# Performance work log

Measured on AMD Instinct MI355X. Metric: run time of the kernel, lower is better.

The kernel has to match this reference:

```python
import jax, jax.numpy as jnp
import numpy as np

B, S, D = 2, 1024, 4096
HQ, HKV, HD = 32, 8, 128
GROUPS = HQ // HKV          # 4
SCALE = HD ** -0.5


def _rope_tables(key):
    # standard RoPE cos/sin tables, non-interleaved (half-split) layout
    inv_freq = 1.0 / (10000.0 ** (jnp.arange(0, HD, 2, dtype=jnp.float32) / HD))  # [HD/2]
    pos = jnp.arange(S, dtype=jnp.float32)                                        # [S]
    freqs = pos[:, None] * inv_freq[None, :]                                      # [S, HD/2]
    emb = jnp.concatenate([freqs, freqs], axis=-1)                                # [S, HD]
    cos = jnp.broadcast_to(jnp.cos(emb)[None], (B, S, HD))
    sin = jnp.broadcast_to(jnp.sin(emb)[None], (B, S, HD))
    return cos, sin


def setup_inputs() -> dict:
    key = jax.random.key(0)
    ks = jax.random.split(key, 6)
    hidden_states = jax.random.normal(ks[0], (B, S, D), dtype=jnp.float32)
    cos_table, sin_table = _rope_tables(ks[1])
    Wq = jax.random.normal(ks[2], (D, HQ * HD), dtype=jnp.float32) * (D ** -0.5)
    Wk = jax.random.normal(ks[3], (D, HKV * HD), dtype=jnp.float32) * (D ** -0.5)
    Wv = jax.random.normal(ks[4], (D, HKV * HD), dtype=jnp.float32) * (D ** -0.5)
    Wo = jax.random.normal(ks[5], (HQ * HD, D), dtype=jnp.float32) * ((HQ * HD) ** -0.5)
    return {"hidden_states": hidden_states, "cos_table": cos_table,
            "sin_table": sin_table, "Wq": Wq, "Wk": Wk, "Wv": Wv, "Wo": Wo}


def _rotate_half(x):
    x1, x2 = jnp.split(x, 2, axis=-1)
    return jnp.concatenate([-x2, x1], axis=-1)


def _apply_rope(x, cos, sin):
    # x: [B, S, H, HD]; cos/sin: [B, S, HD] broadcast across heads
    c = cos[:, :, None, :]
    s = sin[:, :, None, :]
    return x * c + _rotate_half(x) * s


def reference(hidden_states, cos_table, sin_table, Wq, Wk, Wv, Wo):
    b, s, _ = hidden_states.shape
    # QKV projections (no bias, Llama-style)
    q = (hidden_states @ Wq).reshape(b, s, HQ, HD)
    k = (hidden_states @ Wk).reshape(b, s, HKV, HD)
    v = (hidden_states @ Wv).reshape(b, s, HKV, HD)
    # fused RoPE on q and k (in [B, S, H, HD] layout, as in source)
    q = _apply_rope(q, cos_table, sin_table)
    k = _apply_rope(k, cos_table, sin_table)
    # -> [B, H, S, HD]
    q = q.transpose(0, 2, 1, 3)
    k = k.transpose(0, 2, 1, 3)
    v = v.transpose(0, 2, 1, 3)
    # GQA repeat_kv: [B, HKV, S, HD] -> [B, HQ, S, HD]
    k = jnp.repeat(k, GROUPS, axis=1)
    v = jnp.repeat(v, GROUPS, axis=1)
    # SDPA, no mask (source calls sdpa without a mask)
    scores = jnp.einsum('bhqd,bhkd->bhqk', q, k) * SCALE
    attn = jax.nn.softmax(scores, axis=-1)
    out = jnp.einsum('bhqk,bhkd->bhqd', attn, v)
    out = out.transpose(0, 2, 1, 3).reshape(b, s, HQ * HD)
    return out @ Wo
```

## Files before the change

### kernel.cpp

```cpp
#include <hip/hip_runtime.h>

#define B_   2
#define S_   1024
#define D_   4096
#define HQ_  32
#define HKV_ 8
#define HD_  128
#define SCALE_ 0.08838834764831845f

typedef unsigned short u16;
typedef __attribute__((ext_vector_type(8))) short s16x8;
typedef __attribute__((ext_vector_type(4))) short s16x4;
typedef __attribute__((ext_vector_type(4))) float f32x4;

#define MFMA(a,b,c) __builtin_amdgcn_mfma_f32_16x16x32_bf16((a),(b),(c),0,0,0)

__device__ __forceinline__ u16 bf16_rne(float x) {
  unsigned u = __float_as_uint(x);
  u += 0x7fffu + ((u >> 16) & 1u);
  return (u16)(u >> 16);
}
__device__ __forceinline__ float bf16_up(u16 h) {
  return __uint_as_float(((unsigned)h) << 16);
}
__device__ __forceinline__ void split2(float x, u16& h, u16& l) {
  h = bf16_rne(x);
  l = bf16_rne(x - bf16_up(h));
}

__device__ __forceinline__ void cvt_hi_lo(float a, float b, unsigned& hi, unsigned& lo) {
  unsigned h, l;
  asm("v_cvt_pk_bf16_f32 %0, %1, %2" : "=v"(h) : "v"(a), "v"(b));
  float ra = __uint_as_float(h << 16);
  float rb = __uint_as_float(h & 0xffff0000u);
  float la = a - ra, lb = b - rb;
  asm("v_cvt_pk_bf16_f32 %0, %1, %2" : "=v"(l) : "v"(la), "v"(lb));
  hi = h; lo = l;
}
__device__ __forceinline__ void pack8(float4 x, float4 y, uint4& h, uint4& l) {
  unsigned h0,h1,h2,h3,l0,l1,l2,l3;
  cvt_hi_lo(x.x, x.y, h0, l0);
  cvt_hi_lo(x.z, x.w, h1, l1);
  cvt_hi_lo(y.x, y.y, h2, l2);
  cvt_hi_lo(y.z, y.w, h3, l3);
  h = make_uint4(h0,h1,h2,h3); l = make_uint4(l0,l1,l2,l3);
}

typedef const __attribute__((address_space(1))) void* gas_ptr;
typedef __attribute__((address_space(3))) void* las_ptr;
__device__ __forceinline__ void gload_lds16(const void* g, void* l) {
  __builtin_amdgcn_global_load_lds((gas_ptr)g, (las_ptr)l, 16, 0, 0);
}

__global__ __launch_bounds__(256) void frag_b2(
    const float* __restrict__ W, u16* __restrict__ dh, u16* __restrict__ dl,
    int N, int n0, int Ntot16, int ntoff)
{
  __shared__ float T[32][68];
  const int kt = blockIdx.x, nbk = blockIdx.y;
  const int tid = threadIdx.x;
#pragma unroll
  for (int rep = 0; rep < 2; ++rep) {
    int idx = tid + rep * 256;
    int row = idx >> 4, c4 = (idx & 15) * 4;
    float4 v = *reinterpret_cast<const float4*>(&W[(size_t)(kt*32 + row) * N + n0 + nbk*64 + c4]);
    *reinterpret_cast<float4*>(&T[row][c4]) = v;
  }
  __syncthreads();
  int c = tid;
  int nt = c >> 6, l = c & 63;
  const size_t base = (((size_t)(kt >> 1) * Ntot16 + ntoff + nbk*4 + nt) * 2 + (kt & 1)) * 512;
  u16 hh[8], ll[8];
#pragma unroll
  for (int j = 0; j < 8; ++j) split2(T[(l >> 4)*8 + j][nt*16 + (l & 15)], hh[j], ll[j]);
  *reinterpret_cast<s16x8*>(&dh[base + (size_t)l * 8]) =
    (s16x8){(short)hh[0],(short)hh[1],(short)hh[2],(short)hh[3],
            (short)hh[4],(short)hh[5],(short)hh[6],(short)hh[7]};
  *reinterpret_cast<s16x8*>(&dl[base + (size_t)l * 8]) =
    (s16x8){(short)ll[0],(short)ll[1],(short)ll[2],(short)ll[3],
            (short)ll[4],(short)ll[5],(short)ll[6],(short)ll[7]};
}

__global__ __launch_bounds__(256) void frag_a(
    const float* __restrict__ src, u16* __restrict__ dh, u16* __restrict__ dl)
{
  __shared__ float T[128][68];
  const int kt = blockIdx.x;
  const int mb = blockIdx.y;
  const int tid = threadIdx.x;
#pragma unroll
  for (int rep = 0; rep < 8; ++rep) {
    int idx = tid + rep * 256;
    int row = idx >> 4, c4 = (idx & 15) * 4;
    float4 v = *reinterpret_cast<const float4*>(&src[(size_t)(mb*128 + row) * 4096 + kt*64 + c4]);
    *reinterpret_cast<float4*>(&T[row][c4]) = v;
  }
  __syncthreads();
#pragma unroll
  for (int rep = 0; rep < 4; ++rep) {
    int c = tid + rep * 256;
    int mt = c >> 7, rem = c & 127, kk = rem >> 6, l = rem & 63;
    u16 hh[8], ll[8];
#pragma unroll
    for (int j = 0; j < 8; ++j)
      split2(T[mt*16 + (l & 15)][kk*32 + (l >> 4)*8 + j], hh[j], ll[j]);
    size_t off = (((size_t)(kt*128 + mb*8 + mt)) * 2 + kk) * 512 + (size_t)l * 8;
    *reinterpret_cast<s16x8*>(&dh[off]) =
      (s16x8){(short)hh[0],(short)hh[1],(short)hh[2],(short)hh[3],
              (short)hh[4],(short)hh[5],(short)hh[6],(short)hh[7]};
    *reinterpret_cast<s16x8*>(&dl[off]) =
      (s16x8){(short)ll[0],(short)ll[1],(short)ll[2],(short)ll[3],
              (short)ll[4],(short)ll[5],(short)ll[6],(short)ll[7]};
  }
}

template<int NF, bool RQ>
__device__ __forceinline__ void gemm128_core(
    const u16* __restrict__ PAh, const u16* __restrict__ PAl,
    const u16* __restrict__ PBh, const u16* __restrict__ PBl,
    float* __restrict__ C0, float* __restrict__ C1, float* __restrict__ C2,
    int ldc0, int Nt16, int mb, int nb, u16* L)
{
  const int tid  = threadIdx.x;
  const int lane = tid & 63;
  const int wid  = tid >> 6;
  const int loff = lane * 8;
  const int wm4  = (wid >> 2) * 4;
  const int wnf  = (wid & 3) * NF;
  constexpr int BNT  = 4 * NF;
  constexpr int NCHW = 2 + NF;

  u16* A0 = L;
  u16* A1 = L + 8192;
  u16* B0 = L + 16384;
  u16* B1 = L + 16384 + BNT*1024;

  f32x4 acc[4][NF];
#pragma unroll
  for (int i = 0; i < 4; ++i)
#pragma unroll
    for (int j = 0; j < NF; ++j) acc[i][j] = (f32x4){0.f,0.f,0.f,0.f};

  const u16* sp[NCHW];
  int   dlo[NCHW];
  int   dadd[NCHW];
  size_t adv2[NCHW];
  const size_t aSlab = 131072;
  const size_t bSlab = (size_t)Nt16 * 1024;
#pragma unroll
  for (int i = 0; i < NCHW; ++i) {
    int c = wid + 8*i;
    if (c < 8) {
      sp[i]  = PAh + (size_t)(mb*8 + c)*1024 + loff;
      dlo[i] = c*512;             dadd[i] = 8192;      adv2[i] = aSlab - 512;
    } else if (c < 16) {
      int m = c - 8;
      sp[i]  = PAl + (size_t)(mb*8 + m)*1024 + loff;
      dlo[i] = 4096 + m*512;      dadd[i] = 8192;      adv2[i] = aSlab - 512;
    } else if (c < 16 + BNT) {
      int n = c - 16;
      sp[i]  = PBh + (size_t)(nb*BNT + n)*1024 + loff;
      dlo[i] = 16384 + n*512;     dadd[i] = BNT*1024;  adv2[i] = bSlab - 512;
    } else {
      int n = c - 16 - BNT;
      sp[i]  = PBl + (size_t)(nb*BNT + n)*1024 + loff;
      dlo[i] = 16384 + BNT*512 + n*512; dadd[i] = BNT*1024; adv2[i] = bSlab - 512;
    }
  }

#pragma unroll
  for (int i = 0; i < NCHW; ++i) {
    gload_lds16(sp[i], L + dlo[i]);
    sp[i] += 512;
  }
  __syncthreads();

  for (int t = 0; t < 128; ++t) {
    u16* la = (t & 1) ? A1 : A0;
    u16* lb = (t & 1) ? B1 : B0;
    if (t < 127) {
      const int p = (t + 1) & 1;
#pragma unroll
      for (int i = 0; i < NCHW; ++i) {
        gload_lds16(sp[i], L + dlo[i] + (p ? dadd[i] : 0));
        sp[i] += p ? adv2[i] : 512;
      }
    }

    s16x8 ah[4], al[4], bh[NF], bl[NF];
#pragma unroll
    for (int mf = 0; mf < 4; ++mf)
      ah[mf] = *reinterpret_cast<const s16x8*>(&la[(wm4+mf)*512 + loff]);
#pragma unroll
    for (int nf = 0; nf < NF; ++nf)
      bh[nf] = *reinterpret_cast<const s16x8*>(&lb[(wnf+nf)*512 + loff]);
    __builtin_amdgcn_s_setprio(1);
#pragma unroll
    for (int nf = 0; nf < NF; ++nf)
#pragma unroll
      for (int mf = 0; mf < 4; ++mf)
        acc[mf][nf] = MFMA(ah[mf], bh[nf], acc[mf][nf]);
    __builtin_amdgcn_s_setprio(0);
#pragma unroll
    for (int mf = 0; mf < 4; ++mf)
      al[mf] = *reinterpret_cast<const s16x8*>(&la[4096 + (wm4+mf)*512 + loff]);
    __builtin_amdgcn_s_setprio(1);
#pragma unroll
    for (int nf = 0; nf < NF; ++nf)
#pragma unroll
      for (int mf = 0; mf < 4; ++mf)
        acc[mf][nf] = MFMA(al[mf], bh[nf], acc[mf][nf]);
    __builtin_amdgcn_s_setprio(0);
#pragma unroll
    for (int nf = 0; nf < NF; ++nf)
      bl[nf] = *reinterpret_cast<const s16x8*>(&lb[BNT*512 + (wnf+nf)*512 + loff]);
    __builtin_amdgcn_s_setprio(1);
#pragma unroll
    for (int nf = 0; nf < NF; ++nf)
#pragma unroll
      for (int mf = 0; mf < 4; ++mf)
        acc[mf][nf] = MFMA(ah[mf], bl[nf], acc[mf][nf]);
    __builtin_amdgcn_s_setprio(0);
    __syncthreads();
  }

  const int lg = lane >> 4, lr = lane & 15;
  const int rowb = mb*128 + (wid >> 2) * 64;
#pragma unroll
  for (int mf = 0; mf < 4; ++mf)
#pragma unroll
    for (int nf = 0; nf < NF; ++nf)
#pragma unroll
      for (int r = 0; r < 4; ++r) {
        int row = rowb + mf*16 + lg*4 + r;
        float v = acc[mf][nf][r];
        int gcol = nb*(NF*64) + (wid & 3)*(NF*16) + nf*16 + lr;
        if constexpr (RQ) {
          if (gcol < 4096)      C0[(size_t)row * 4096 + gcol] = v;
          else if (gcol < 5120) C1[(size_t)row * 1024 + (gcol - 4096)] = v;
          else                  C2[(size_t)row * 1024 + (gcol - 5120)] = v;
        } else {
          C0[(size_t)row * ldc0 + gcol] = v;
        }
      }
}

__global__ __launch_bounds__(512, 4) void gemm_qkv3(
    const u16* __restrict__ XAh, const u16* __restrict__ XAl,
    const u16* __restrict__ WBh, const u16* __restrict__ WBl,
    float* __restrict__ qb, float* __restrict__ kb, float* __restrict__ vb)
{
  __shared__ __attribute__((aligned(16))) u16 L[40960];
  int id = blockIdx.x;
  int xcd = id & 7, c = id >> 3;
  int nb = xcd * 4 + (c >> 4);
  int mb = c & 15;
  gemm128_core<3, true>(XAh, XAl, WBh, WBl, qb, kb, vb, 0, 384, mb, nb, L);
}

__global__ __launch_bounds__(512, 4) void gemm_out3(
    const u16* __restrict__ ABh, const u16* __restrict__ ABl,
    const u16* __restrict__ WOh, const u16* __restrict__ WOl,
    float* __restrict__ outp)
{
  __shared__ __attribute__((aligned(16))) u16 L[32768];
  int id = blockIdx.x;
  int xcd = id & 7, c = id >> 3;
  int nb = xcd * 4 + (c >> 4);
  int mb = c & 15;
  gemm128_core<2, false>(ABh, ABl, WOh, WOl, outp, nullptr, nullptr,
                         4096, 256, mb, nb, L);
}

template<int NF, bool RQ>
__device__ __forceinline__ void gemm256_core(
    const u16* __restrict__ PAh, const u16* __restrict__ PAl,
    const u16* __restrict__ PBh, const u16* __restrict__ PBl,
    float* __restrict__ C0, float* __restrict__ C1, float* __restrict__ C2,
    int ldc0, int Nt16, int mb, int nb, int k0, int nk, u16* L)
{
  const int tid  = threadIdx.x;
  const int lane = tid & 63;
  const int wid  = tid >> 6;
  const int loff = lane * 8;
  const int wm8  = (wid >> 2) * 8;
  const int wnf  = (wid & 3) * NF;

  u16* A0 = L;
  u16* A1 = L + 16384;
  u16* B0 = L + 32768;
  u16* B1 = L + 32768 + NF*4096;

  f32x4 acc[8][NF];
#pragma unroll
  for (int i = 0; i < 8; ++i)
#pragma unroll
    for (int j = 0; j < NF; ++j) acc[i][j] = (f32x4){0.f,0.f,0.f,0.f};

  auto STAGE = [&](int t, u16* la_, u16* lb_) {
    const int kt64 = t >> 1, kk = t & 1;
    const size_t aSlab = (size_t)kt64 * 131072;
    const size_t bSlab = (size_t)kt64 * ((size_t)Nt16 * 1024);
    const int NCH = 32 + 8*NF;
#pragma unroll
    for (int c = wid; c < NCH; c += 8) {
      const u16* src; u16* dst;
      if (c < 16) {
        src = PAh + aSlab + (((size_t)(mb*16 + c))*2 + kk)*512;
        dst = la_ + c*512;
      } else if (c < 32) {
        int m = c - 16;
        src = PAl + aSlab + (((size_t)(mb*16 + m))*2 + kk)*512;
        dst = la_ + 8192 + m*512;
      } else if (c < 32 + 4*NF) {
        int n = c - 32;
        src = PBh + bSlab + (((size_t)(nb*4*NF + n))*2 + kk)*512;
        dst = lb_ + n*512;
      } else {
        int n = c - 32 - 4*NF;
        src = PBl + bSlab + (((size_t)(nb*4*NF + n))*2 + kk)*512;
        dst = lb_ + NF*2048 + n*512;
      }
      gload_lds16(src + loff, dst);
    }
  };

  STAGE(k0, (k0 & 1) ? A1 : A0, (k0 & 1) ? B1 : B0);
  __syncthreads();

  for (int t = k0; t < k0 + nk; ++t) {
    u16* la = (t & 1) ? A1 : A0;
    u16* lb = (t & 1) ? B1 : B0;
    if (t + 1 < k0 + nk)
      STAGE(t + 1, (t & 1) ? A0 : A1, (t & 1) ? B0 : B1);

    s16x8 ah[8], al[8], bh[NF], bl[NF];
#pragma unroll
    for (int mf = 0; mf < 8; ++mf)
      ah[mf] = *reinterpret_cast<const s16x8*>(&la[(wm8+mf)*512 + loff]);
#pragma unroll
    for (int nf = 0; nf < NF; ++nf)
      bh[nf] = *reinterpret_cast<const s16x8*>(&lb[(wnf+nf)*512 + loff]);
    __builtin_amdgcn_s_setprio(1);
#pragma unroll
    for (int nf = 0; nf < NF; ++nf)
#pragma unroll
      for (int mf = 0; mf < 8; ++mf)
        acc[mf][nf] = MFMA(ah[mf], bh[nf], acc[mf][nf]);
    __builtin_amdgcn_s_setprio(0);
#pragma unroll
    for (int mf = 0; mf < 8; ++mf)
      al[mf] = *reinterpret_cast<const s16x8*>(&la[8192 + (wm8+mf)*512 + loff]);
    __builtin_amdgcn_s_setprio(1);
#pragma unroll
    for (int nf = 0; nf < NF; ++nf)
#pragma unroll
      for (int mf = 0; mf < 8; ++mf)
        acc[mf][nf] = MFMA(al[mf], bh[nf], acc[mf][nf]);
    __builtin_amdgcn_s_setprio(0);
#pragma unroll
    for (int nf = 0; nf < NF; ++nf)
      bl[nf] = *reinterpret_cast<const s16x8*>(&lb[NF*2048 + (wnf+nf)*512 + loff]);
    __builtin_amdgcn_s_setprio(1);
#pragma unroll
    for (int nf = 0; nf < NF; ++nf)
#pragma unroll
      for (int mf = 0; mf < 8; ++mf)
        acc[mf][nf] = MFMA(ah[mf], bl[nf], acc[mf][nf]);
    __builtin_amdgcn_s_setprio(0);
    __syncthreads();
  }

  const int lg = lane >> 4, lr = lane & 15;
  const int rowb = mb*256 + (wid >> 2) * 128;
#pragma unroll
  for (int mf = 0; mf < 8; ++mf)
#pragma unroll
    for (int nf = 0; nf < NF; ++nf)
#pragma unroll
      for (int r = 0; r < 4; ++r) {
        int row = rowb + mf*16 + lg*4 + r;
        float v = acc[mf][nf][r];
        if constexpr (RQ) {
          int gcol = nb*(NF*64) + (wid & 3)*(NF*16) + nf*16 + lr;
          if (gcol < 4096)      C0[(size_t)row * 4096 + gcol] = v;
          else if (gcol < 5120) C1[(size_t)row * 1024 + (gcol - 4096)] = v;
          else                  C2[(size_t)row * 1024 + (gcol - 5120)] = v;
        } else {
          int col = nb*(NF*64) + (wid & 3)*(NF*16) + nf*16 + lr;
          C0[(size_t)row * ldc0 + col] = v;
        }
      }
}

__global__ __launch_bounds__(512) void gemm_qkv2(
    const u16* __restrict__ XAh, const u16* __restrict__ XAl,
    const u16* __restrict__ WA,
    float* __restrict__ qb, float* __restrict__ kb, float* __restrict__ vb)
{
  __shared__ __attribute__((aligned(16))) u16 L[65536];
  int id = blockIdx.x;
  int swz = (id & 7) * 24 + (id >> 3);
  const u16 *Bh, *Bl; float* C; int ldc, Nt16, mb, nb;
  if (swz < 128)      { Bh = WA;          Bl = WA+16777216; C = qb; ldc = 4096; Nt16 = 256; mb = swz & 7;  nb = swz >> 3; }
  else if (swz < 160) { int u = swz-128; Bh = WA+33554432; Bl = WA+37748736; C = kb; ldc = 1024; Nt16 = 64; mb = u & 7; nb = u >> 3; }
  else                { int u = swz-160; Bh = WA+41943040; Bl = WA+46137344; C = vb; ldc = 1024; Nt16 = 64; mb = u & 7; nb = u >> 3; }
  gemm256_core<4, false>(XAh, XAl, Bh, Bl, C, nullptr, nullptr, ldc, Nt16, mb, nb, 0, 128, L);
}

__global__ __launch_bounds__(512) void gemm_out2(
    const u16* __restrict__ ABh, const u16* __restrict__ ABl,
    const u16* __restrict__ WOh, const u16* __restrict__ WOl,
    float* __restrict__ outp, float* __restrict__ c2)
{
  __shared__ __attribute__((aligned(16))) u16 L[65536];
  int id = blockIdx.x;
  int swz = (id & 7) * 32 + (id >> 3);
  int u = swz & 127, s = swz >> 7;
  int mb = u & 7, nb = u >> 3;
  gemm256_core<4, false>(ABh, ABl, WOh, WOl, s ? c2 : outp, nullptr, nullptr,
                         4096, 256, mb, nb, s*64, 64, L);
}

__global__ __launch_bounds__(256) void add_out(
    float* __restrict__ o, const float* __restrict__ c2)
{
  int i = blockIdx.x * 256 + threadIdx.x;
  float4 a = reinterpret_cast<float4*>(o)[i];
  float4 b = reinterpret_cast<const float4*>(c2)[i];
  a.x += b.x; a.y += b.y; a.z += b.z; a.w += b.w;
  reinterpret_cast<float4*>(o)[i] = a;
}

__global__ __launch_bounds__(256) void frag_kv(
    const float* __restrict__ kb, const float* __restrict__ vb,
    const float* __restrict__ cosT, const float* __restrict__ sinT,
    u16* __restrict__ KFh, u16* __restrict__ KFl,
    u16* __restrict__ VFh, u16* __restrict__ VFl)
{
  __shared__ float T[32][132];
  const int bid  = blockIdx.x;
  const int isV  = bid >> 9;
  const int bkvh = (bid >> 5) & 15;
  const int chnk = bid & 31;
  const int tid  = threadIdx.x;
  const int b    = bkvh >> 3, kvh = bkvh & 7;

  const float* src = isV ? vb : kb;
  {
    int r0 = tid >> 5, c4 = (tid & 31) * 4;
    float sgn = (c4 < 64) ? -1.f : 1.f;
#pragma unroll
    for (int it = 0; it < 4; ++it) {
      int row = r0 + it * 8;
      int srow = chnk*32 + row;
      const float* rp = &src[(((size_t)(b * S_ + srow)) * HKV_ + kvh) * HD_];
      float4 v = *reinterpret_cast<const float4*>(rp + c4);
      if (!isV) {
        float4 p  = *reinterpret_cast<const float4*>(rp + (c4 ^ 64));
        float4 cc = *reinterpret_cast<const float4*>(&cosT[((size_t)(b*S_ + srow))*HD_ + c4]);
        float4 ss = *reinterpret_cast<const float4*>(&sinT[((size_t)(b*S_ + srow))*HD_ + c4]);
        v.x = v.x*cc.x + sgn*p.x*ss.x;
        v.y = v.y*cc.y + sgn*p.y*ss.y;
        v.z = v.z*cc.z + sgn*p.z*ss.z;
        v.w = v.w*cc.w + sgn*p.w*ss.w;
      }
      *reinterpret_cast<float4*>(&T[row][c4]) = v;
    }
  }
  __syncthreads();
#pragma unroll
  for (int rep = 0; rep < 2; ++rep) {
    int c2 = tid + rep * 256;
    int l = c2 & 63;
    u16 hh[8], ll[8];
    if (!isV) {
      int f = c2 >> 6, st_loc = f >> 2, dt = f & 3;
#pragma unroll
      for (int j = 0; j < 8; ++j)
        split2(T[st_loc*16 + (l & 15)][dt*32 + (l >> 4)*8 + j], hh[j], ll[j]);
      size_t off = ((size_t)bkvh*64 + chnk*2) * 2048 + (size_t)c2 * 8;
      *reinterpret_cast<s16x8*>(&KFh[off]) =
        (s16x8){(short)hh[0],(short)hh[1],(short)hh[2],(short)hh[3],
                (short)hh[4],(short)hh[5],(short)hh[6],(short)hh[7]};
      *reinterpret_cast<s16x8*>(&KFl[off]) =
        (s16x8){(short)ll[0],(short)ll[1],(short)ll[2],(short)ll[3],
                (short)ll[4],(short)ll[5],(short)ll[6],(short)ll[7]};
    } else {
      int dt16 = c2 >> 6;
#pragma unroll
      for (int j = 0; j < 8; ++j)
        split2(T[(l >> 4)*8 + j][dt16*16 + (l & 15)], hh[j], ll[j]);
      size_t off = ((size_t)bkvh*32 + chnk) * 4096 + (size_t)c2 * 8;
      *reinterpret_cast<s16x8*>(&VFh[off]) =
        (s16x8){(short)hh[0],(short)hh[1],(short)hh[2],(short)hh[3],
                (short)hh[4],(short)hh[5],(short)hh[6],(short)hh[7]};
      *reinterpret_cast<s16x8*>(&VFl[off]) =
        (s16x8){(short)ll[0],(short)ll[1],(short)ll[2],(short)ll[3],
                (short)ll[4],(short)ll[5],(short)ll[6],(short)ll[7]};
    }
  }
}

__global__ __launch_bounds__(512) void attn3(
    const float* __restrict__ qb,
    const float* __restrict__ cosT, const float* __restrict__ sinT,
    const u16* __restrict__ KFh, const u16* __restrict__ KFl,
    const u16* __restrict__ VFh, const u16* __restrict__ VFl,
    float* __restrict__ ob)
{
  __shared__ __attribute__((aligned(16))) u16 Klds[16384];
  __shared__ __attribute__((aligned(16))) u16 Vlds[16384];
  __shared__ u16 Ph[8][16][68], Pl[8][16][68];

  const int tid  = threadIdx.x;
  const int lane = tid & 63;
  const int wid  = tid >> 6;
  const int lr   = lane & 15;
  const int lg   = lane >> 4;
  const int loff = lane * 8;
  const int qt   = blockIdx.x;
  const int bh   = blockIdx.y;
  const int b    = bh >> 5, h = bh & 31;
  const int bkvh = b * 8 + (h >> 2);

  s16x8 qh[4], ql[4];
  {
    const int qrow = qt * 128 + wid * 16 + lr;
    const float* qp = qb + ((size_t)((b * S_ + qrow) * HQ_ + h)) * HD_;
    const float* cp = cosT + ((size_t)(b * S_ + qrow)) * HD_;
    const float* sp = sinT + ((size_t)(b * S_ + qrow)) * HD_;
#pragma unroll
    for (int kc = 0; kc < 4; ++kc) {
      const int d0 = kc * 32 + lg * 8;
      const float sgn = (d0 < 64) ? -1.f : 1.f;
      float4 v0 = *reinterpret_cast<const float4*>(qp + d0);
      float4 v1 = *reinterpret_cast<const float4*>(qp + d0 + 4);
      float4 p0 = *reinterpret_cast<const float4*>(qp + (d0 ^ 64));
      float4 p1 = *reinterpret_cast<const float4*>(qp + (d0 ^ 64) + 4);
      float4 c0 = *reinterpret_cast<const float4*>(cp + d0);
      float4 c1 = *reinterpret_cast<const float4*>(cp + d0 + 4);
      float4 s0 = *reinterpret_cast<const float4*>(sp + d0);
      float4 s1 = *reinterpret_cast<const float4*>(sp + d0 + 4);
      float4 r0, r1;
      r0.x = v0.x*c0.x + sgn*p0.x*s0.x;  r0.y = v0.y*c0.y + sgn*p0.y*s0.y;
      r0.z = v0.z*c0.z + sgn*p0.z*s0.z;  r0.w = v0.w*c0.w + sgn*p0.w*s0.w;
      r1.x = v1.x*c1.x + sgn*p1.x*s1.x;  r1.y = v1.y*c1.y + sgn*p1.y*s1.y;
      r1.z = v1.z*c1.z + sgn*p1.z*s1.z;  r1.w = v1.w*c1.w + sgn*p1.w*s1.w;
      uint4 h4, l4; pack8(r0, r1, h4, l4);
      qh[kc] = *reinterpret_cast<s16x8*>(&h4);
      ql[kc] = *reinterpret_cast<s16x8*>(&l4);
    }
  }

  f32x4 acc_o[8];
#pragma unroll
  for (int df = 0; df < 8; ++df) acc_o[df] = (f32x4){0.f, 0.f, 0.f, 0.f};
  float m_run[4] = {-1e30f, -1e30f, -1e30f, -1e30f};
  float l_run[4] = {0.f, 0.f, 0.f, 0.f};

  const u16* gKh = KFh + (size_t)bkvh * 131072;
  const u16* gKl = KFl + (size_t)bkvh * 131072;
  const u16* gVh = VFh + (size_t)bkvh * 131072;
  const u16* gVl = VFl + (size_t)bkvh * 131072;

#pragma unroll
  for (int i = 0; i < 4; ++i) {
    int idx = wid * 4 + i;
    const u16* src = (idx < 16) ? (gKh + idx*512) : (gKl + (idx-16)*512);
    u16* dst = Klds + ((idx < 16) ? idx*512 : 8192 + (idx-16)*512);
    gload_lds16(src + loff, dst);
  }
  __syncthreads();

  for (int t = 0; t < 16; ++t) {
#pragma unroll
    for (int i = 0; i < 4; ++i) {
      int idx = wid * 4 + i;
      const u16* src = (idx < 16) ? (gVh + t*8192 + idx*512)
                                  : (gVl + t*8192 + (idx-16)*512);
      u16* dst = Vlds + ((idx < 16) ? idx*512 : 8192 + (idx-16)*512);
      gload_lds16(src + loff, dst);
    }

    f32x4 accs[4];
#pragma unroll
    for (int nf = 0; nf < 4; ++nf) {
      accs[nf] = (f32x4){0.f, 0.f, 0.f, 0.f};
      s16x8 kh8[4], kl8[4];
#pragma unroll
      for (int kc = 0; kc < 4; ++kc) {
        kh8[kc] = *reinterpret_cast<const s16x8*>(&Klds[nf*2048 + kc*512 + loff]);
        kl8[kc] = *reinterpret_cast<const s16x8*>(&Klds[8192 + nf*2048 + kc*512 + loff]);
      }
#pragma unroll
      for (int kc = 0; kc < 4; ++kc) {
        accs[nf] = MFMA(qh[kc], kh8[kc], accs[nf]);
        accs[nf] = MFMA(ql[kc], kh8[kc], accs[nf]);
        accs[nf] = MFMA(qh[kc], kl8[kc], accs[nf]);
      }
    }
#pragma unroll
    for (int nf = 0; nf < 4; ++nf) accs[nf] *= SCALE_;

    float corr[4], rsum[4];
#pragma unroll
    for (int r = 0; r < 4; ++r) {
      float t0 = fmaxf(fmaxf(accs[0][r], accs[1][r]), fmaxf(accs[2][r], accs[3][r]));
      t0 = fmaxf(t0, __shfl_xor(t0, 1));
      t0 = fmaxf(t0, __shfl_xor(t0, 2));
      t0 = fmaxf(t0, __shfl_xor(t0, 4));
      t0 = fmaxf(t0, __shfl_xor(t0, 8));
      float mnew = fmaxf(m_run[r], t0);
      corr[r] = __expf(m_run[r] - mnew);
      m_run[r] = mnew;
      rsum[r] = 0.f;
    }
#pragma unroll
    for (int nf = 0; nf < 4; ++nf)
#pragma unroll
      for (int r = 0; r < 4; ++r) {
        float p = __expf(accs[nf][r] - m_run[r]);
        rsum[r] += p;
        u16 ph, pl;
        split2(p, ph, pl);
        Ph[wid][lg*4 + r][nf*16 + lr] = ph;
        Pl[wid][lg*4 + r][nf*16 + lr] = pl;
      }
#pragma unroll
    for (int r = 0; r < 4; ++r) {
      float s = rsum[r];
      s += __shfl_xor(s, 1); s += __shfl_xor(s, 2);
      s += __shfl_xor(s, 4); s += __shfl_xor(s, 8);
      l_run[r] = l_run[r] * corr[r] + s;
    }
#pragma unroll
    for (int df = 0; df < 8; ++df)
#pragma unroll
      for (int r = 0; r < 4; ++r) acc_o[df][r] *= corr[r];

    __syncthreads();

    if (t < 15) {
#pragma unroll
      for (int i = 0; i < 4; ++i) {
        int idx = wid * 4 + i;
        const u16* src = (idx < 16) ? (gKh + (t+1)*8192 + idx*512)
                                    : (gKl + (t+1)*8192 + (idx-16)*512);
        u16* dst = Klds + ((idx < 16) ? idx*512 : 8192 + (idx-16)*512);
        gload_lds16(src + loff, dst);
      }
    }

    s16x8 pa_h[2], pa_l[2];
#pragma unroll
    for (int kc = 0; kc < 2; ++kc) {
      pa_h[kc] = *reinterpret_cast<const s16x8*>(&Ph[wid][lr][kc*32 + lg*8]);
      pa_l[kc] = *reinterpret_cast<const s16x8*>(&Pl[wid][lr][kc*32 + lg*8]);
    }
#pragma unroll
    for (int df = 0; df < 8; ++df) {
      s16x8 vh8[2], vl8[2];
#pragma unroll
      for (int kc = 0; kc < 2; ++kc) {
        vh8[kc] = *reinterpret_cast<const s16x8*>(&Vlds[kc*4096 + df*512 + loff]);
        vl8[kc] = *reinterpret_cast<const s16x8*>(&Vlds[8192 + kc*4096 + df*512 + loff]);
      }
#pragma unroll
      for (int kc = 0; kc < 2; ++kc) {
        acc_o[df] = MFMA(pa_h[kc], vh8[kc], acc_o[df]);
        acc_o[df] = MFMA(pa_l[kc], vh8[kc], acc_o[df]);
        acc_o[df] = MFMA(pa_h[kc], vl8[kc], acc_o[df]);
      }
    }
    __syncthreads();
  }

  float inv_l[4];
#pragma unroll
  for (int r = 0; r < 4; ++r) inv_l[r] = 1.f / l_run[r];
#pragma unroll
  for (int df = 0; df < 8; ++df)
#pragma unroll
    for (int r = 0; r < 4; ++r) {
      int row = qt * 128 + wid * 16 + lg * 4 + r;
      ob[((size_t)((b * S_ + row) * HQ_ + h)) * HD_ + df*16 + lr] = acc_o[df][r] * inv_l[r];
    }
}

extern "C" void kernel_launch(void* const* d_in, const int* in_sizes, int n_in,
                              void* d_out, int out_size, void* d_ws, size_t ws_size,
                              hipStream_t stream)
{
  const float* hs   = (const float*)d_in[0];
  const float* cosT = (const float*)d_in[1];
  const float* sinT = (const float*)d_in[2];
  const float* Wq   = (const float*)d_in[3];
  const float* Wk   = (const float*)d_in[4];
  const float* Wv   = (const float*)d_in[5];
  const float* Wo   = (const float*)d_in[6];
  float* out = (float*)d_out;

  float* qb = (float*)d_ws;
  float* kb = qb + 8388608;
  float* vb = kb + 2097152;
  float* ab = vb + 2097152;
  u16*   FR = (u16*)(ab + 8388608);

  const size_t WS212 = 222298112ULL;

  if (ws_size >= WS212) {
    u16* XAh = FR;
    u16* XAl = FR + 8388608;
    u16* WBh = FR + 16777216;
    u16* WBl = FR + 41943040;
    u16* KFh = FR + 16777216;
    u16* KFl = FR + 18874368;
    u16* VFh = FR + 20971520;
    u16* VFl = FR + 23068672;
    u16* WOh = FR + 25165824;
    u16* WOl = FR + 41943040;

    frag_a<<<dim3(64,16), 256, 0, stream>>>(hs, XAh, XAl);
    frag_b2<<<dim3(128,64), 256, 0, stream>>>(Wq, WBh, WBl, 4096, 0, 384, 0);
    frag_b2<<<dim3(128,16), 256, 0, stream>>>(Wk, WBh, WBl, 1024, 0, 384, 256);
    frag_b2<<<dim3(128,16), 256, 0, stream>>>(Wv, WBh, WBl, 1024, 0, 384, 320);
    gemm_qkv3<<<512, 512, 0, stream>>>(XAh, XAl, WBh, WBl, qb, kb, vb);
    frag_kv<<<1024, 256, 0, stream>>>(kb, vb, cosT, sinT, KFh, KFl, VFh, VFl);
    frag_b2<<<dim3(128,64), 256, 0, stream>>>(Wo, WOh, WOl, 4096, 0, 256, 0);
    attn3<<<dim3(8, 64), 512, 0, stream>>>(qb, cosT, sinT, KFh, KFl, VFh, VFl, ab);
    frag_a<<<dim3(64,16), 256, 0, stream>>>(ab, XAh, XAl);
    gemm_out3<<<512, 512, 0, stream>>>(XAh, XAl, WOh, WOl, out);
  } else {
    u16* XAh = FR;
    u16* XAl = FR + 8388608;
    u16* WA  = FR + 16777216;
    frag_a<<<dim3(64,16), 256, 0, stream>>>(hs, XAh, XAl);
    frag_b2<<<dim3(128,64), 256, 0, stream>>>(Wq, WA,           WA+16777216, 4096, 0, 256, 0);
    frag_b2<<<dim3(128,16), 256, 0, stream>>>(Wk, WA+33554432,  WA+37748736, 1024, 0, 64, 0);
    frag_b2<<<dim3(128,16), 256, 0, stream>>>(Wv, WA+41943040,  WA+46137344, 1024, 0, 64, 0);
    gemm_qkv2<<<192, 512, 0, stream>>>(XAh, XAl, WA, qb, kb, vb);
    frag_kv<<<1024, 256, 0, stream>>>(kb, vb, cosT, sinT,
                                      WA, WA+2097152, WA+4194304, WA+6291456);
    frag_b2<<<dim3(128,64), 256, 0, stream>>>(Wo, WA+8388608, WA+25165824, 4096, 0, 256, 0);
    attn3<<<dim3(8, 64), 512, 0, stream>>>(qb, cosT, sinT,
                                           WA, WA+2097152, WA+4194304, WA+6291456, ab);
    frag_a<<<dim3(64,16), 256, 0, stream>>>(ab, XAh, XAl);
    gemm_out2<<<256, 512, 0, stream>>>(XAh, XAl, WA+8388608, WA+25165824, out, qb);
    add_out<<<8192, 256, 0, stream>>>(out, qb);
  }
}
```

Baseline: 648.3 us.

## Add smaller-tile attention kernel with 32-key steps and pairwise bf16 split packing

Introduces attn4, which handles 64 query rows per block with 4 waves and iterates over 32-key chunks using half-size LDS buffers. This gives more blocks (1024 instead of 512) and higher occupancy via launch_bounds(256,3), at the cost of twice as many loop iterations and barriers. The fragment conversion kernels now convert pairs of floats into packed hi/lo bf16 words with cvt_hi_lo and store them as uint4 instead of assembling eight shorts. attn4 replaces attn3 in the primary launch path, while the fallback path still uses attn3.

```diff
diff --git a/kernel.cpp b/kernel.cpp
--- a/kernel.cpp
+++ b/kernel.cpp
@@ -70,15 +70,13 @@
   int c = tid;
   int nt = c >> 6, l = c & 63;
   const size_t base = (((size_t)(kt >> 1) * Ntot16 + ntoff + nbk*4 + nt) * 2 + (kt & 1)) * 512;
-  u16 hh[8], ll[8];
-#pragma unroll
-  for (int j = 0; j < 8; ++j) split2(T[(l >> 4)*8 + j][nt*16 + (l & 15)], hh[j], ll[j]);
-  *reinterpret_cast<s16x8*>(&dh[base + (size_t)l * 8]) =
-    (s16x8){(short)hh[0],(short)hh[1],(short)hh[2],(short)hh[3],
-            (short)hh[4],(short)hh[5],(short)hh[6],(short)hh[7]};
-  *reinterpret_cast<s16x8*>(&dl[base + (size_t)l * 8]) =
-    (s16x8){(short)ll[0],(short)ll[1],(short)ll[2],(short)ll[3],
-            (short)ll[4],(short)ll[5],(short)ll[6],(short)ll[7]};
+  const int r0 = (l >> 4) * 8, cc = nt*16 + (l & 15);
+  unsigned hh4[4], ll4[4];
+#pragma unroll
+  for (int p = 0; p < 4; ++p)
+    cvt_hi_lo(T[r0 + 2*p][cc], T[r0 + 2*p + 1][cc], hh4[p], ll4[p]);
+  *reinterpret_cast<uint4*>(&dh[base + (size_t)l * 8]) = make_uint4(hh4[0],hh4[1],hh4[2],hh4[3]);
+  *reinterpret_cast<uint4*>(&dl[base + (size_t)l * 8]) = make_uint4(ll4[0],ll4[1],ll4[2],ll4[3]);
 }
 
 __global__ __launch_bounds__(256) void frag_a(
@@ -100,17 +98,14 @@
   for (int rep = 0; rep < 4; ++rep) {
     int c = tid + rep * 256;
     int mt = c >> 7, rem = c & 127, kk = rem >> 6, l = rem & 63;
-    u16 hh[8], ll[8];
-#pragma unroll
-    for (int j = 0; j < 8; ++j)
-      split2(T[mt*16 + (l & 15)][kk*32 + (l >> 4)*8 + j], hh[j], ll[j]);
+    const int rr = mt*16 + (l & 15), c0 = kk*32 + (l >> 4)*8;
+    unsigned hh4[4], ll4[4];
+#pragma unroll
+    for (int p = 0; p < 4; ++p)
+      cvt_hi_lo(T[rr][c0 + 2*p], T[rr][c0 + 2*p + 1], hh4[p], ll4[p]);
     size_t off = (((size_t)(kt*128 + mb*8 + mt)) * 2 + kk) * 512 + (size_t)l * 8;
-    *reinterpret_cast<s16x8*>(&dh[off]) =
-      (s16x8){(short)hh[0],(short)hh[1],(short)hh[2],(short)hh[3],
-              (short)hh[4],(short)hh[5],(short)hh[6],(short)hh[7]};
-    *reinterpret_cast<s16x8*>(&dl[off]) =
-      (s16x8){(short)ll[0],(short)ll[1],(short)ll[2],(short)ll[3],
-              (short)ll[4],(short)ll[5],(short)ll[6],(short)ll[7]};
+    *reinterpret_cast<uint4*>(&dh[off]) = make_uint4(hh4[0],hh4[1],hh4[2],hh4[3]);
+    *reinterpret_cast<uint4*>(&dl[off]) = make_uint4(ll4[0],ll4[1],ll4[2],ll4[3]);
   }
 }
 
@@ -473,45 +468,39 @@
   for (int rep = 0; rep < 2; ++rep) {
     int c2 = tid + rep * 256;
     int l = c2 & 63;
-    u16 hh[8], ll[8];
+    unsigned hh4[4], ll4[4];
     if (!isV) {
       int f = c2 >> 6, st_loc = f >> 2, dt = f & 3;
-#pragma unroll
-      for (int j = 0; j < 8; ++j)
-        split2(T[st_loc*16 + (l & 15)][dt*32 + (l >> 4)*8 + j], hh[j], ll[j]);
+      const int rr = st_loc*16 + (l & 15), c0 = dt*32 + (l >> 4)*8;
+#pragma unroll
+      for (int p = 0; p < 4; ++p)
+        cvt_hi_lo(T[rr][c0 + 2*p], T[rr][c0 + 2*p + 1], hh4[p], ll4[p]);
       size_t off = ((size_t)bkvh*64 + chnk*2) * 2048 + (size_t)c2 * 8;
-      *reinterpret_cast<s16x8*>(&KFh[off]) =
-        (s16x8){(short)hh[0],(short)hh[1],(short)hh[2],(short)hh[3],
-                (short)hh[4],(short)hh[5],(short)hh[6],(short)hh[7]};
-      *reinterpret_cast<s16x8*>(&KFl[off]) =
-        (s16x8){(short)ll[0],(short)ll[1],(short)ll[2],(short)ll[3],
-                (short)ll[4],(short)ll[5],(short)ll[6],(short)ll[7]};
+      *reinterpret_cast<uint4*>(&KFh[off]) = make_uint4(hh4[0],hh4[1],hh4[2],hh4[3]);
+      *reinterpret_cast<uint4*>(&KFl[off]) = make_uint4(ll4[0],ll4[1],ll4[2],ll4[3]);
     } else {
       int dt16 = c2 >> 6;
-#pragma unroll
-      for (int j = 0; j < 8; ++j)
-        split2(T[(l >> 4)*8 + j][dt16*16 + (l & 15)], hh[j], ll[j]);
+      const int r0 = (l >> 4)*8, cc = dt16*16 + (l & 15);
+#pragma unroll
+      for (int p = 0; p < 4; ++p)
+        cvt_hi_lo(T[r0 + 2*p][cc], T[r0 + 2*p + 1][cc], hh4[p], ll4[p]);
       size_t off = ((size_t)bkvh*32 + chnk) * 4096 + (size_t)c2 * 8;
-      *reinterpret_cast<s16x8*>(&VFh[off]) =
-        (s16x8){(short)hh[0],(short)hh[1],(short)hh[2],(short)hh[3],
-                (short)hh[4],(short)hh[5],(short)hh[6],(short)hh[7]};
-      *reinterpret_cast<s16x8*>(&VFl[off]) =
-        (s16x8){(short)ll[0],(short)ll[1],(short)ll[2],(short)ll[3],
-                (short)ll[4],(short)ll[5],(short)ll[6],(short)ll[7]};
-    }
-  }
-}
-
-__global__ __launch_bounds__(512) void attn3(
+      *reinterpret_cast<uint4*>(&VFh[off]) = make_uint4(hh4[0],hh4[1],hh4[2],hh4[3]);
+      *reinterpret_cast<uint4*>(&VFl[off]) = make_uint4(ll4[0],ll4[1],ll4[2],ll4[3]);
+    }
+  }
+}
+
+__global__ __launch_bounds__(256, 3) void attn4(
     const float* __restrict__ qb,
     const float* __restrict__ cosT, const float* __restrict__ sinT,
     const u16* __restrict__ KFh, const u16* __restrict__ KFl,
     const u16* __restrict__ VFh, const u16* __restrict__ VFl,
     float* __restrict__ ob)
 {
-  __shared__ __attribute__((aligned(16))) u16 Klds[16384];
-  __shared__ __attribute__((aligned(16))) u16 Vlds[16384];
-  __shared__ u16 Ph[8][16][68], Pl[8][16][68];
+  __shared__ __attribute__((aligned(16))) u16 Klds[8192];
+  __shared__ __attribute__((aligned(16))) u16 Vlds[8192];
+  __shared__ u16 Ph[4][16][36], Pl[4][16][36];
 
   const int tid  = threadIdx.x;
   const int lane = tid & 63;
@@ -526,7 +515,7 @@
 
   s16x8 qh[4], ql[4];
   {
-    const int qrow = qt * 128 + wid * 16 + lr;
+    const int qrow = qt * 64 + wid * 16 + lr;
     const float* qp = qb + ((size_t)((b * S_ + qrow) * HQ_ + h)) * HD_;
     const float* cp = cosT + ((size_t)(b * S_ + qrow)) * HD_;
     const float* sp = sinT + ((size_t)(b * S_ + qrow)) * HD_;
@@ -565,6 +554,176 @@
   const u16* gVl = VFl + (size_t)bkvh * 131072;
 
 #pragma unroll
+  for (int i = 0; i < 2; ++i) {
+    int c = wid * 2 + i;
+    gload_lds16(gKh + c*512 + loff, Klds + c*512);
+    gload_lds16(gKl + c*512 + loff, Klds + 4096 + c*512);
+  }
+  __syncthreads();
+
+  for (int t = 0; t < 32; ++t) {
+#pragma unroll
+    for (int i = 0; i < 2; ++i) {
+      int c = wid * 2 + i;
+      gload_lds16(gVh + t*4096 + c*512 + loff, Vlds + c*512);
+      gload_lds16(gVl + t*4096 + c*512 + loff, Vlds + 4096 + c*512);
+    }
+
+    f32x4 accs[2];
+#pragma unroll
+    for (int nf = 0; nf < 2; ++nf) {
+      accs[nf] = (f32x4){0.f, 0.f, 0.f, 0.f};
+      s16x8 kh8[4], kl8[4];
+#pragma unroll
+      for (int kc = 0; kc < 4; ++kc) {
+        kh8[kc] = *reinterpret_cast<const s16x8*>(&Klds[nf*2048 + kc*512 + loff]);
+        kl8[kc] = *reinterpret_cast<const s16x8*>(&Klds[4096 + nf*2048 + kc*512 + loff]);
+      }
+#pragma unroll
+      for (int kc = 0; kc < 4; ++kc) {
+        accs[nf] = MFMA(qh[kc], kh8[kc], accs[nf]);
+        accs[nf] = MFMA(ql[kc], kh8[kc], accs[nf]);
+        accs[nf] = MFMA(qh[kc], kl8[kc], accs[nf]);
+      }
+    }
+#pragma unroll
+    for (int nf = 0; nf < 2; ++nf) accs[nf] *= SCALE_;
+
+    float corr[4], rsum[4];
+#pragma unroll
+    for (int r = 0; r < 4; ++r) {
+      float t0 = fmaxf(accs[0][r], accs[1][r]);
+      t0 = fmaxf(t0, __shfl_xor(t0, 1));
+      t0 = fmaxf(t0, __shfl_xor(t0, 2));
+      t0 = fmaxf(t0, __shfl_xor(t0, 4));
+      t0 = fmaxf(t0, __shfl_xor(t0, 8));
+      float mnew = fmaxf(m_run[r], t0);
+      corr[r] = __expf(m_run[r] - mnew);
+      m_run[r] = mnew;
+      rsum[r] = 0.f;
+    }
+#pragma unroll
+    for (int nf = 0; nf < 2; ++nf)
+#pragma unroll
+      for (int r = 0; r < 4; ++r) {
+        float p = __expf(accs[nf][r] - m_run[r]);
+        rsum[r] += p;
+        u16 ph, pl;
+        split2(p, ph, pl);
+        Ph[wid][lg*4 + r][nf*16 + lr] = ph;
+        Pl[wid][lg*4 + r][nf*16 + lr] = pl;
+      }
+#pragma unroll
+    for (int r = 0; r < 4; ++r) {
+      float s = rsum[r];
+      s += __shfl_xor(s, 1); s += __shfl_xor(s, 2);
+      s += __shfl_xor(s, 4); s += __shfl_xor(s, 8);
+      l_run[r] = l_run[r] * corr[r] + s;
+    }
+#pragma unroll
+    for (int df = 0; df < 8; ++df)
+#pragma unroll
+      for (int r = 0; r < 4; ++r) acc_o[df][r] *= corr[r];
+
+    __syncthreads();
+
+    if (t < 31) {
+#pragma unroll
+      for (int i = 0; i < 2; ++i) {
+        int c = wid * 2 + i;
+        gload_lds16(gKh + (t+1)*4096 + c*512 + loff, Klds + c*512);
+        gload_lds16(gKl + (t+1)*4096 + c*512 + loff, Klds + 4096 + c*512);
+      }
+    }
+
+    s16x8 pa_h = *reinterpret_cast<const s16x8*>(&Ph[wid][lr][lg*8]);
+    s16x8 pa_l = *reinterpret_cast<const s16x8*>(&Pl[wid][lr][lg*8]);
+#pragma unroll
+    for (int df = 0; df < 8; ++df) {
+      s16x8 vh8 = *reinterpret_cast<const s16x8*>(&Vlds[df*512 + loff]);
+      s16x8 vl8 = *reinterpret_cast<const s16x8*>(&Vlds[4096 + df*512 + loff]);
+      acc_o[df] = MFMA(pa_h, vh8, acc_o[df]);
+      acc_o[df] = MFMA(pa_l, vh8, acc_o[df]);
+      acc_o[df] = MFMA(pa_h, vl8, acc_o[df]);
+    }
+    __syncthreads();
+  }
+
+  float inv_l[4];
+#pragma unroll
+  for (int r = 0; r < 4; ++r) inv_l[r] = 1.f / l_run[r];
+#pragma unroll
+  for (int df = 0; df < 8; ++df)
+#pragma unroll
+    for (int r = 0; r < 4; ++r) {
+      int row = qt * 64 + wid * 16 + lg * 4 + r;
+      ob[((size_t)((b * S_ + row) * HQ_ + h)) * HD_ + df*16 + lr] = acc_o[df][r] * inv_l[r];
+    }
+}
+
+__global__ __launch_bounds__(512) void attn3(
+    const float* __restrict__ qb,
+    const float* __restrict__ cosT, const float* __restrict__ sinT,
+    const u16* __restrict__ KFh, const u16* __restrict__ KFl,
+    const u16* __restrict__ VFh, const u16* __restrict__ VFl,
+    float* __restrict__ ob)
+{
+  __shared__ __attribute__((aligned(16))) u16 Klds[16384];
+  __shared__ __attribute__((aligned(16))) u16 Vlds[16384];
+  __shared__ u16 Ph[8][16][68], Pl[8][16][68];
+
+  const int tid  = threadIdx.x;
+  const int lane = tid & 63;
+  const int wid  = tid >> 6;
+  const int lr   = lane & 15;
+  const int lg   = lane >> 4;
+  const int loff = lane * 8;
+  const int qt   = blockIdx.x;
+  const int bh   = blockIdx.y;
+  const int b    = bh >> 5, h = bh & 31;
+  const int bkvh = b * 8 + (h >> 2);
+
+  s16x8 qh[4], ql[4];
+  {
+    const int qrow = qt * 128 + wid * 16 + lr;
+    const float* qp = qb + ((size_t)((b * S_ + qrow) * HQ_ + h)) * HD_;
+    const float* cp = cosT + ((size_t)(b * S_ + qrow)) * HD_;
+    const float* sp = sinT + ((size_t)(b * S_ + qrow)) * HD_;
+#pragma unroll
+    for (int kc = 0; kc < 4; ++kc) {
+      const int d0 = kc * 32 + lg * 8;
+      const float sgn = (d0 < 64) ? -1.f : 1.f;
+      float4 v0 = *reinterpret_cast<const float4*>(qp + d0);
+      float4 v1 = *reinterpret_cast<const float4*>(qp + d0 + 4);
+      float4 p0 = *reinterpret_cast<const float4*>(qp + (d0 ^ 64));
+      float4 p1 = *reinterpret_cast<const float4*>(qp + (d0 ^ 64) + 4);
+      float4 c0 = *reinterpret_cast<const float4*>(cp + d0);
+      float4 c1 = *reinterpret_cast<const float4*>(cp + d0 + 4);
+      float4 s0 = *reinterpret_cast<const float4*>(sp + d0);
+      float4 s1 = *reinterpret_cast<const float4*>(sp + d0 + 4);
+      float4 r0, r1;
+      r0.x = v0.x*c0.x + sgn*p0.x*s0.x;  r0.y = v0.y*c0.y + sgn*p0.y*s0.y;
+      r0.z = v0.z*c0.z + sgn*p0.z*s0.z;  r0.w = v0.w*c0.w + sgn*p0.w*s0.w;
+      r1.x = v1.x*c1.x + sgn*p1.x*s1.x;  r1.y = v1.y*c1.y + sgn*p1.y*s1.y;
+      r1.z = v1.z*c1.z + sgn*p1.z*s1.z;  r1.w = v1.w*c1.w + sgn*p1.w*s1.w;
+      uint4 h4, l4; pack8(r0, r1, h4, l4);
+      qh[kc] = *reinterpret_cast<s16x8*>(&h4);
+      ql[kc] = *reinterpret_cast<s16x8*>(&l4);
+    }
+  }
+
+  f32x4 acc_o[8];
+#pragma unroll
+  for (int df = 0; df < 8; ++df) acc_o[df] = (f32x4){0.f, 0.f, 0.f, 0.f};
+  float m_run[4] = {-1e30f, -1e30f, -1e30f, -1e30f};
+  float l_run[4] = {0.f, 0.f, 0.f, 0.f};
+
+  const u16* gKh = KFh + (size_t)bkvh * 131072;
+  const u16* gKl = KFl + (size_t)bkvh * 131072;
+  const u16* gVh = VFh + (size_t)bkvh * 131072;
+  const u16* gVl = VFl + (size_t)bkvh * 131072;
+
+#pragma unroll
   for (int i = 0; i < 4; ++i) {
     int idx = wid * 4 + i;
     const u16* src = (idx < 16) ? (gKh + idx*512) : (gKl + (idx-16)*512);
@@ -728,7 +887,7 @@
     gemm_qkv3<<<512, 512, 0, stream>>>(XAh, XAl, WBh, WBl, qb, kb, vb);
     frag_kv<<<1024, 256, 0, stream>>>(kb, vb, cosT, sinT, KFh, KFl, VFh, VFl);
     frag_b2<<<dim3(128,64), 256, 0, stream>>>(Wo, WOh, WOl, 4096, 0, 256, 0);
-    attn3<<<dim3(8, 64), 512, 0, stream>>>(qb, cosT, sinT, KFh, KFl, VFh, VFl, ab);
+    attn4<<<dim3(16, 64), 256, 0, stream>>>(qb, cosT, sinT, KFh, KFl, VFh, VFl, ab);
     frag_a<<<dim3(64,16), 256, 0, stream>>>(ab, XAh, XAl);
     gemm_out3<<<512, 512, 0, stream>>>(XAh, XAl, WOh, WOl, out);
   } else {
```

After: 679.2 us. +4.8%, slower.
